# Kernel optimization log

Hardware: AMD Instinct MI355X
Metric: run time of the kernel (lower is better)

The kernel has to match this reference:

```python
import jax, jax.numpy as jnp
import numpy as np
from jax import lax

B, T = 16, 8192
CIN, HALF, F = 2, 1, 256
KS, NL, NB, TB = 3, 3, 10, 5.0
PROJ = HALF * (3 * NB - 1)


def setup_inputs() -> dict:
    key = jax.random.key(0)
    ks = jax.random.split(key, 16)
    inp = {
        'x': jax.random.normal(ks[0], (B, T, CIN), dtype=jnp.float32),
        'x_mask': jnp.ones((B, T, 1), dtype=jnp.float32),
        'w_pre': jax.random.normal(ks[1], (HALF, F)) * 0.1,
        'b_pre': jnp.zeros((F,)),
        'dw_k': jax.random.normal(ks[2], (NL, KS, 1, F)) * 0.1,   # depthwise kernels [L,k,1,C]
        'dw_b': jnp.zeros((NL, F)),
        'w11': jax.random.normal(ks[3], (NL, F, F)) * 0.05,
        'b11': jnp.zeros((NL, F)),
        'ln1_g': jnp.ones((NL, F)), 'ln1_b': jnp.zeros((NL, F)),
        'ln2_g': jnp.ones((NL, F)), 'ln2_b': jnp.zeros((NL, F)),
        'w_proj': jax.random.normal(ks[4], (F, PROJ)) * 0.05,
        'b_proj': jnp.zeros((PROJ,)),
    }
    return inp


def _layer_norm(x, g, b, eps=1e-5):
    m = jnp.mean(x, axis=-1, keepdims=True)
    v = jnp.mean(jnp.square(x - m), axis=-1, keepdims=True)
    return (x - m) * lax.rsqrt(v + eps) * g + b


def _rq_spline(x, uw, uh, ud, tail_bound, mbw=1e-3, mbh=1e-3, md=1e-3):
    # x: [B,c,T]; uw,uh: [B,c,T,K]; ud: [B,c,T,K-1]. tails='linear'.
    K = uw.shape[-1]
    const = float(np.log(np.expm1(1.0 - md)))  # boundary derivative == 1
    ud = jnp.pad(ud, [(0, 0)] * (ud.ndim - 1) + [(1, 1)], constant_values=const)
    inside = (x >= -tail_bound) & (x <= tail_bound)

    w = jax.nn.softmax(uw, axis=-1)
    w = mbw + (1.0 - mbw * K) * w
    cw = jnp.pad(jnp.cumsum(w, axis=-1), [(0, 0)] * (w.ndim - 1) + [(1, 0)])
    cw = 2.0 * tail_bound * cw - tail_bound
    cw = cw.at[..., 0].set(-tail_bound).at[..., -1].set(tail_bound)
    w = jnp.diff(cw, axis=-1)

    hgt = jax.nn.softmax(uh, axis=-1)
    hgt = mbh + (1.0 - mbh * K) * hgt
    ch = jnp.pad(jnp.cumsum(hgt, axis=-1), [(0, 0)] * (hgt.ndim - 1) + [(1, 0)])
    ch = 2.0 * tail_bound * ch - tail_bound
    ch = ch.at[..., 0].set(-tail_bound).at[..., -1].set(tail_bound)
    hgt = jnp.diff(ch, axis=-1)

    d = md + jax.nn.softplus(ud)  # [B,c,T,K+1]

    xc = jnp.clip(x, -tail_bound, tail_bound)
    idx = jnp.clip(jnp.sum((xc[..., None] >= cw).astype(jnp.int32), axis=-1) - 1, 0, K - 1)

    def g1(a, i):
        return jnp.take_along_axis(a, i[..., None], axis=-1)[..., 0]

    icw, ibw = g1(cw, idx), g1(w, idx)
    ich, ibh = g1(ch, idx), g1(hgt, idx)
    delta = ibh / ibw
    dk, dk1 = g1(d, idx), g1(d, idx + 1)

    th = (xc - icw) / ibw
    th1m = th * (1.0 - th)
    denom = delta + (dk + dk1 - 2.0 * delta) * th1m
    num = ibh * (delta * th * th + dk * th1m)
    yv = ich + num / denom
    dnum = jnp.square(delta) * (dk1 * th * th + 2.0 * delta * th1m + dk * jnp.square(1.0 - th))
    lad = jnp.log(dnum) - 2.0 * jnp.log(denom)

    y = jnp.where(inside, yv, x)
    lad = jnp.where(inside, lad, jnp.zeros_like(lad))
    return y, lad


def reference(x, x_mask, w_pre, b_pre, dw_k, dw_b, w11, b11,
              ln1_g, ln1_b, ln2_g, ln2_b, w_proj, b_proj):
    half = w_pre.shape[0]
    F_ = w_pre.shape[1]
    nl, ks = dw_k.shape[0], dw_k.shape[1]
    x0, x1 = x[..., :half], x[..., half:]

    h = x0 @ w_pre + b_pre  # pre 1x1 conv, [B,T,F]
    for i in range(nl):  # DDSConv
        dil = ks ** i
        y = lax.conv_general_dilated(h * x_mask, dw_k[i], (1,), 'SAME',
                                     rhs_dilation=(dil,),
                                     dimension_numbers=('NWC', 'WIO', 'NWC'),
                                     feature_group_count=F_) + dw_b[i]
        y = jax.nn.gelu(_layer_norm(y, ln1_g[i], ln1_b[i]), approximate=False)
        y = y @ w11[i] + b11[i]
        y = jax.nn.gelu(_layer_norm(y, ln2_g[i], ln2_b[i]), approximate=False)
        h = h + y
    h = h * x_mask
    h = (h @ w_proj + b_proj) * x_mask  # [B,T,half*(3*NB-1)]

    b_, t_ = x.shape[0], x.shape[1]
    nb = (h.shape[-1] // half + 1) // 3
    h = h.reshape(b_, t_, half, 3 * nb - 1).transpose(0, 2, 1, 3)  # [B,half,T,3NB-1]
    x1t = jnp.swapaxes(x1, 1, 2)  # [B,half,T]

    scale = 1.0 / np.sqrt(F_)
    uw = h[..., :nb] * scale
    uh = h[..., nb:2 * nb] * scale
    ud = h[..., 2 * nb:]

    y1, lad = _rq_spline(x1t, uw, uh, ud, TB)
    x1o = jnp.swapaxes(y1, 1, 2)           # [B,T,half]
    lad_t = jnp.swapaxes(lad, 1, 2)        # [B,T,half]

    xo = jnp.concatenate([x0, x1o], axis=-1) * x_mask
    logdet = jnp.sum(lad_t * x_mask, axis=(2, 1))
    return xo, logdet
```

## Files before the change

### kernel.cpp

```cpp
#include <hip/hip_runtime.h>
#include <hip/hip_bf16.h>
#include <cmath>

#define BB 16
#define TT 8192
#define MM (BB*TT)
#define FF 256
#define TBF 5.0f
#define PROJN 29

typedef __attribute__((ext_vector_type(8))) short short8;
typedef __attribute__((ext_vector_type(4))) float f32x4;

__device__ __forceinline__ float gelu_exact(float x){
    const float z  = x*0.70710678118654752440f;
    const float az = fabsf(z);
    const float t  = __builtin_amdgcn_rcpf(fmaf(0.3275911f, az, 1.0f));
    float p = fmaf(1.061405429f, t, -1.453152027f);
    p = fmaf(p, t, 1.421413741f);
    p = fmaf(p, t, -0.284496736f);
    p = fmaf(p, t, 0.254829592f);
    p = p*t;
    const float e  = __expf(-az*az);
    const float r  = fmaf(-p, e, 1.0f);
    return 0.5f*x*(1.0f + copysignf(r, z));
}
__device__ __forceinline__ float softplusf_(float v){
    return fmaxf(v,0.0f) + log1pf(__expf(-fabsf(v)));
}
__device__ __forceinline__ unsigned pack2bf(float a, float b){
    __hip_bfloat16 ha = __float2bfloat16(a);
    __hip_bfloat16 hb = __float2bfloat16(b);
    const unsigned ua = *reinterpret_cast<const unsigned short*>(&ha);
    const unsigned ub = *reinterpret_cast<const unsigned short*>(&hb);
    return ua | (ub<<16);
}
__device__ __forceinline__ float bf2f(unsigned short u){
    unsigned v = ((unsigned)u)<<16;
    return *reinterpret_cast<float*>(&v);
}
__device__ __forceinline__ float4 unpack4(uint2 q){
    float4 f;
    f.x = bf2f((unsigned short)(q.x&0xffff)); f.y = bf2f((unsigned short)(q.x>>16));
    f.z = bf2f((unsigned short)(q.y&0xffff)); f.w = bf2f((unsigned short)(q.y>>16));
    return f;
}

__global__ __launch_bounds__(256) void wprep_kernel(
    const float* __restrict__ w11, const float* __restrict__ wproj,
    __hip_bfloat16* __restrict__ wimg, __hip_bfloat16* __restrict__ wpimg)
{
    if(blockIdx.x < 24){
        const int layer = blockIdx.x>>3, kc = blockIdx.x&7;
        const float* __restrict__ w = w11 + (size_t)layer*FF*FF;
        __hip_bfloat16* __restrict__ o = wimg + (size_t)layer*81920 + kc*10240;
        for(int i=threadIdx.x; i<10240; i+=256){
            const int n = i/40, kp = i - n*40;
            const float v = (kp<32) ? w[(size_t)(kc*32+kp)*FF + n] : 0.0f;
            o[i] = __float2bfloat16(v);
        }
    } else {
        const int kc = blockIdx.x - 24;
        __hip_bfloat16* __restrict__ o = wpimg + (size_t)kc*1280;
        for(int i=threadIdx.x; i<1280; i+=256){
            const int n = i/40, kp = i - n*40;
            const float v = (kp<32 && n<PROJN) ? wproj[(size_t)(kc*32+kp)*PROJN + n] : 0.0f;
            o[i] = __float2bfloat16(v);
        }
    }
}

__global__ __launch_bounds__(256,4) void layer_kernel(
    const __hip_bfloat16* __restrict__ hbin, __hip_bfloat16* __restrict__ hbout,
    const float* __restrict__ xsrc,
    const float* __restrict__ w_pre, const float* __restrict__ b_pre,
    const float* __restrict__ mask,
    const float* __restrict__ dwk, const float* __restrict__ dwb,
    const float* __restrict__ g1, const float* __restrict__ b1,
    const __hip_bfloat16* __restrict__ wimgL, const float* __restrict__ b11,
    const float* __restrict__ g2, const float* __restrict__ b2,
    const int dil, const int pre_mode)
{
    __shared__ __hip_bfloat16 ytile[32][264];
    __shared__ __hip_bfloat16 hstash[32][268];
    __shared__ float redS[32][4];
    __shared__ float redQ[32][4];
    __shared__ float stat[32][2];

    const int tid  = threadIdx.x;
    const int wave = tid>>6, lane = tid&63;
    const int l15  = lane&15, qq = lane>>4;

    int bid = blockIdx.x;
    bid = (bid&7)*((int)gridDim.x>>3) + (bid>>3);
    const int m0 = bid*32;
    const int b  = m0/TT;
    const int t0 = m0 - b*TT;
    const float* __restrict__ mrow = mask + (size_t)b*TT;

    const int f0 = lane*4;
    const float4 k0 = *(const float4*)&dwk[f0];
    const float4 k1 = *(const float4*)&dwk[FF+f0];
    const float4 k2 = *(const float4*)&dwk[2*FF+f0];
    const float4 cb = *(const float4*)&dwb[f0];
    const float4 g1v= *(const float4*)&g1[f0];
    const float4 b1v= *(const float4*)&b1[f0];
    float4 wp4, bp4;
    if(pre_mode){ wp4 = *(const float4*)&w_pre[f0]; bp4 = *(const float4*)&b_pre[f0]; }

    #pragma unroll 4
    for(int rr=0; rr<8; ++rr){
        const int r = wave*8+rr;
        const int m = m0+r, t = t0+r;
        const int okl = (t>=dil)   ? 1 : 0;
        const int okr = (t+dil<TT) ? 1 : 0;
        const int ml  = m - dil*okl;
        const int mr  = m + dil*okr;
        const float mkc = mrow[t];
        const float mkl = mrow[t - dil*okl] * (float)okl;
        const float mkr = mrow[t + dil*okr] * (float)okr;
        float4 hc, hl, hr;
        uint2 hcraw;
        if(pre_mode){
            const float xc_ = xsrc[(size_t)m *2];
            const float xl_ = xsrc[(size_t)ml*2];
            const float xr_ = xsrc[(size_t)mr*2];
            hc.x=fmaf(xc_,wp4.x,bp4.x); hc.y=fmaf(xc_,wp4.y,bp4.y);
            hc.z=fmaf(xc_,wp4.z,bp4.z); hc.w=fmaf(xc_,wp4.w,bp4.w);
            hl.x=fmaf(xl_,wp4.x,bp4.x); hl.y=fmaf(xl_,wp4.y,bp4.y);
            hl.z=fmaf(xl_,wp4.z,bp4.z); hl.w=fmaf(xl_,wp4.w,bp4.w);
            hr.x=fmaf(xr_,wp4.x,bp4.x); hr.y=fmaf(xr_,wp4.y,bp4.y);
            hr.z=fmaf(xr_,wp4.z,bp4.z); hr.w=fmaf(xr_,wp4.w,bp4.w);
            hcraw = make_uint2(pack2bf(hc.x,hc.y), pack2bf(hc.z,hc.w));
        } else {
            hcraw          = *(const uint2*)&hbin[(size_t)m *FF + f0];
            const uint2 ql = *(const uint2*)&hbin[(size_t)ml*FF + f0];
            const uint2 qr = *(const uint2*)&hbin[(size_t)mr*FF + f0];
            hc = unpack4(hcraw); hl = unpack4(ql); hr = unpack4(qr);
        }
        *(uint2*)&hstash[r][f0] = hcraw;
        float4 a;
        a.x = fmaf(hc.x*mkc, k1.x, cb.x);
        a.y = fmaf(hc.y*mkc, k1.y, cb.y);
        a.z = fmaf(hc.z*mkc, k1.z, cb.z);
        a.w = fmaf(hc.w*mkc, k1.w, cb.w);
        a.x = fmaf(hl.x*mkl, k0.x, a.x);
        a.y = fmaf(hl.y*mkl, k0.y, a.y);
        a.z = fmaf(hl.z*mkl, k0.z, a.z);
        a.w = fmaf(hl.w*mkl, k0.w, a.w);
        a.x = fmaf(hr.x*mkr, k2.x, a.x);
        a.y = fmaf(hr.y*mkr, k2.y, a.y);
        a.z = fmaf(hr.z*mkr, k2.z, a.z);
        a.w = fmaf(hr.w*mkr, k2.w, a.w);
        float s  = a.x+a.y+a.z+a.w;
        float sq = fmaf(a.x,a.x, fmaf(a.y,a.y, fmaf(a.z,a.z, a.w*a.w)));
        #pragma unroll
        for(int o=32;o>0;o>>=1){
            s  += __shfl_xor(s,o,64);
            sq += __shfl_xor(sq,o,64);
        }
        const float mean = s*(1.0f/FF);
        const float var  = fmaf(-mean, mean, sq*(1.0f/FF));
        const float rs = rsqrtf(var + 1e-5f);
        const float y0 = gelu_exact(fmaf((a.x-mean)*rs, g1v.x, b1v.x));
        const float y1 = gelu_exact(fmaf((a.y-mean)*rs, g1v.y, b1v.y));
        const float y2 = gelu_exact(fmaf((a.z-mean)*rs, g1v.z, b1v.z));
        const float y3 = gelu_exact(fmaf((a.w-mean)*rs, g1v.w, b1v.w));
        *(uint2*)&ytile[r][f0] = make_uint2(pack2bf(y0,y1), pack2bf(y2,y3));
    }

    __syncthreads();

    const int wc = wave*64;
    f32x4 acc[2][4];
    #pragma unroll
    for(int mf=0;mf<2;++mf)
        #pragma unroll
        for(int nf=0;nf<4;++nf)
            acc[mf][nf] = (f32x4){0.f,0.f,0.f,0.f};

    #pragma unroll
    for(int kc=0;kc<8;++kc){
        short8 bfv[4];
        #pragma unroll
        for(int nf=0;nf<4;++nf)
            bfv[nf] = *(const short8*)&wimgL[(size_t)kc*10240 + (wc+nf*16+l15)*40 + qq*8];
        short8 af[2];
        #pragma unroll
        for(int mf=0;mf<2;++mf)
            af[mf] = *(const short8*)&ytile[mf*16+l15][kc*32 + qq*8];
        #pragma unroll
        for(int nf=0;nf<4;++nf)
            #pragma unroll
            for(int mf=0;mf<2;++mf)
                acc[mf][nf] = __builtin_amdgcn_mfma_f32_16x16x32_bf16(af[mf], bfv[nf], acc[mf][nf], 0,0,0);
    }

    float b11c[4], g2c[4], b2c[4];
    #pragma unroll
    for(int nf=0;nf<4;++nf){
        const int col = wc + nf*16 + l15;
        b11c[nf]=b11[col]; g2c[nf]=g2[col]; b2c[nf]=b2[col];
    }
    #pragma unroll
    for(int mf=0;mf<2;++mf){
        #pragma unroll
        for(int rg=0;rg<4;++rg){
            float s=0.f, sq=0.f;
            #pragma unroll
            for(int nf=0;nf<4;++nf){
                const float v = acc[mf][nf][rg] + b11c[nf];
                s += v; sq = fmaf(v,v,sq);
            }
            #pragma unroll
            for(int o=1;o<16;o<<=1){ s += __shfl_xor(s,o,64); sq += __shfl_xor(sq,o,64); }
            if(l15==0){
                const int row = mf*16 + qq*4 + rg;
                redS[row][wave]=s; redQ[row][wave]=sq;
            }
        }
    }
    __syncthreads();
    if(tid < 32){
        const float s  = redS[tid][0]+redS[tid][1]+redS[tid][2]+redS[tid][3];
        const float q2 = redQ[tid][0]+redQ[tid][1]+redQ[tid][2]+redQ[tid][3];
        const float mean = s*(1.0f/FF);
        const float var  = fmaf(-mean, mean, q2*(1.0f/FF));
        stat[tid][0]=mean; stat[tid][1]=rsqrtf(var+1e-5f);
    }
    __syncthreads();
    #pragma unroll
    for(int mf=0;mf<2;++mf){
        #pragma unroll
        for(int rg=0;rg<4;++rg){
            const int row = mf*16 + qq*4 + rg;
            const float mean = stat[row][0], rs = stat[row][1];
            const size_t gbase = (size_t)(m0+row)*FF;
            #pragma unroll
            for(int nf=0;nf<4;++nf){
                const int col = wc + nf*16 + l15;
                const float v  = acc[mf][nf][rg] + b11c[nf];
                const float yn = fmaf((v-mean)*rs, g2c[nf], b2c[nf]);
                const float res = bf2f(*reinterpret_cast<const unsigned short*>(&hstash[row][col]));
                hbout[gbase+col] = __float2bfloat16(res + gelu_exact(yn));
            }
        }
    }
}

__global__ __launch_bounds__(256,4) void proj_kernel(
    const __hip_bfloat16* __restrict__ hbin, const float* __restrict__ mask,
    const __hip_bfloat16* __restrict__ wpimg, const float* __restrict__ bproj,
    float* __restrict__ P)
{
    __shared__ __hip_bfloat16 ytile[64][264];
    const int tid = threadIdx.x;
    const int wave = tid>>6, lane = tid&63;
    const int l15 = lane&15, qq = lane>>4;
    const int m0 = blockIdx.x*64;
    const int f0 = lane*4;

    #pragma unroll 4
    for(int rr=0; rr<16; ++rr){
        const int r = wave*16+rr;
        const int m = m0+r;
        const float mk = mask[m];
        const float4 hc = unpack4(*(const uint2*)&hbin[(size_t)m*FF + f0]);
        *(uint2*)&ytile[r][f0] = make_uint2(pack2bf(hc.x*mk, hc.y*mk), pack2bf(hc.z*mk, hc.w*mk));
    }
    __syncthreads();

    const int rh = (wave&1)*32, wc2 = (wave>>1)*16;
    f32x4 acc[2];
    acc[0] = (f32x4){0.f,0.f,0.f,0.f};
    acc[1] = (f32x4){0.f,0.f,0.f,0.f};
    #pragma unroll
    for(int kc=0;kc<8;++kc){
        const short8 bfv = *(const short8*)&wpimg[(size_t)kc*1280 + (wc2+l15)*40 + qq*8];
        #pragma unroll
        for(int mf=0;mf<2;++mf){
            const short8 af = *(const short8*)&ytile[rh+mf*16+l15][kc*32 + qq*8];
            acc[mf] = __builtin_amdgcn_mfma_f32_16x16x32_bf16(af, bfv, acc[mf], 0,0,0);
        }
    }
    const int col = wc2 + l15;
    const float bp = (col<PROJN)? bproj[col] : 0.0f;
    #pragma unroll
    for(int mf=0;mf<2;++mf){
        #pragma unroll
        for(int rg=0;rg<4;++rg){
            const int row = rh + mf*16 + qq*4 + rg;
            const float mk = mask[m0+row];
            P[(size_t)(m0+row)*32 + col] = (acc[mf][rg] + bp)*mk;
        }
    }
}

__global__ __launch_bounds__(256) void spline_kernel(
    const float* __restrict__ P, const float* __restrict__ x,
    const float* __restrict__ mask, float* __restrict__ out,
    float* __restrict__ logdet)
{
    const int tid = threadIdx.x;
    const int m = blockIdx.x*256 + tid;
    float p[32];
    #pragma unroll
    for(int j=0;j<8;++j) ((float4*)p)[j] = ((const float4*)P)[(size_t)m*8+j];
    const float x0 = x[(size_t)m*2];
    const float x1 = x[(size_t)m*2+1];
    const float mk = mask[m];
    const float sc = 0.0625f;

    float cw[11], ch[11], d[11];
    {
        float mx=-1e30f;
        #pragma unroll
        for(int j=0;j<10;++j) mx = fmaxf(mx, p[j]);
        float e[10]; float se=0.f;
        #pragma unroll
        for(int j=0;j<10;++j){ e[j]=__expf((p[j]-mx)*sc); se+=e[j]; }
        const float inv = __fdividef(1.0f, se);
        float cum=0.f;
        cw[0]=-TBF;
        #pragma unroll
        for(int j=0;j<10;++j){ cum += fmaf(0.99f, e[j]*inv, 0.001f); cw[j+1]=fmaf(2.0f*TBF,cum,-TBF); }
        cw[10]=TBF;
    }
    {
        float mx=-1e30f;
        #pragma unroll
        for(int j=0;j<10;++j) mx = fmaxf(mx, p[10+j]);
        float e[10]; float se=0.f;
        #pragma unroll
        for(int j=0;j<10;++j){ e[j]=__expf((p[10+j]-mx)*sc); se+=e[j]; }
        const float inv = __fdividef(1.0f, se);
        float cum=0.f;
        ch[0]=-TBF;
        #pragma unroll
        for(int j=0;j<10;++j){ cum += fmaf(0.99f, e[j]*inv, 0.001f); ch[j+1]=fmaf(2.0f*TBF,cum,-TBF); }
        ch[10]=TBF;
    }
    d[0]=1.0f; d[10]=1.0f;
    #pragma unroll
    for(int k=1;k<10;++k) d[k] = 0.001f + softplusf_(p[19+k]);

    const bool inside = (x1>=-TBF)&&(x1<=TBF);
    const float xc = fminf(fmaxf(x1,-TBF),TBF);

    float icw=cw[0], ibw=cw[1]-cw[0], ich=ch[0], ibh=ch[1]-ch[0], dk=d[0], dk1=d[1];
    #pragma unroll
    for(int j=1;j<10;++j){
        const bool sel = (xc>=cw[j]);
        icw = sel? cw[j]      : icw;
        ibw = sel? cw[j+1]-cw[j] : ibw;
        ich = sel? ch[j]      : ich;
        ibh = sel? ch[j+1]-ch[j] : ibh;
        dk  = sel? d[j]       : dk;
        dk1 = sel? d[j+1]     : dk1;
    }

    const float delta = __fdividef(ibh, ibw);
    const float th = __fdividef(xc-icw, ibw);
    const float th1m = th*(1.0f-th);
    const float denom = fmaf(fmaf(-2.0f,delta,dk+dk1), th1m, delta);
    const float num = ibh*fmaf(delta*th, th, dk*th1m);
    const float yv = ich + __fdividef(num, denom);
    const float omt = 1.0f-th;
    const float dnum = delta*delta*(dk1*th*th + 2.0f*delta*th1m + dk*omt*omt);
    const float lad = __logf(dnum) - 2.0f*__logf(denom);
    const float y1 = inside? yv : x1;
    const float lv = inside? lad : 0.0f;

    out[(size_t)m*2]   = x0*mk;
    out[(size_t)m*2+1] = y1*mk;

    __shared__ float red[256];
    red[tid]=lv*mk;
    __syncthreads();
    #pragma unroll
    for(int s=128;s>0;s>>=1){ if(tid<s) red[tid]+=red[tid+s]; __syncthreads(); }
    if(tid==0) atomicAdd(&logdet[blockIdx.x>>5], red[0]);
}

extern "C" void kernel_launch(void* const* d_in, const int* in_sizes, int n_in,
                              void* d_out, int out_size, void* d_ws, size_t ws_size,
                              hipStream_t stream)
{
    const float* x      = (const float*)d_in[0];
    const float* mask   = (const float*)d_in[1];
    const float* w_pre  = (const float*)d_in[2];
    const float* b_pre  = (const float*)d_in[3];
    const float* dw_k   = (const float*)d_in[4];
    const float* dw_b   = (const float*)d_in[5];
    const float* w11    = (const float*)d_in[6];
    const float* b11    = (const float*)d_in[7];
    const float* ln1g   = (const float*)d_in[8];
    const float* ln1b   = (const float*)d_in[9];
    const float* ln2g   = (const float*)d_in[10];
    const float* ln2b   = (const float*)d_in[11];
    const float* w_proj = (const float*)d_in[12];
    const float* b_proj = (const float*)d_in[13];

    const size_t hbytes_f32 = (size_t)MM*FF*4;
    __hip_bfloat16* h0 = (__hip_bfloat16*)d_ws;
    __hip_bfloat16* h1 = h0 + (size_t)MM*FF;
    float* P = (float*)d_ws;
    float* outp   = (float*)d_out;
    float* logdet = outp + (size_t)MM*2;

    __hip_bfloat16* wimg;
    if(ws_size >= 2*hbytes_f32 + 3*163840 + 20480)
        wimg = (__hip_bfloat16*)((char*)d_ws + 2*hbytes_f32);
    else
        wimg = (__hip_bfloat16*)d_out;
    __hip_bfloat16* wpimg = wimg + (size_t)3*81920;

    wprep_kernel<<<32, 256, 0, stream>>>(w11, w_proj, wimg, wpimg);

    layer_kernel<<<MM/32, 256, 0, stream>>>(
        (const __hip_bfloat16*)nullptr, h1, x, w_pre, b_pre, mask,
        dw_k, dw_b, ln1g, ln1b, wimg, b11, ln2g, ln2b, 1, 1);
    layer_kernel<<<MM/32, 256, 0, stream>>>(
        h1, h0, x, w_pre, b_pre, mask,
        dw_k + (size_t)3*FF, dw_b + (size_t)FF,
        ln1g + (size_t)FF, ln1b + (size_t)FF,
        wimg + (size_t)81920, b11 + (size_t)FF,
        ln2g + (size_t)FF, ln2b + (size_t)FF, 3, 0);
    layer_kernel<<<MM/32, 256, 0, stream>>>(
        h0, h1, x, w_pre, b_pre, mask,
        dw_k + (size_t)6*FF, dw_b + (size_t)2*FF,
        ln1g + (size_t)2*FF, ln1b + (size_t)2*FF,
        wimg + (size_t)2*81920, b11 + (size_t)2*FF,
        ln2g + (size_t)2*FF, ln2b + (size_t)2*FF, 9, 0);

    proj_kernel<<<MM/64, 256, 0, stream>>>(h1, mask, wpimg, b_proj, P);

    hipMemsetAsync(logdet, 0, BB*sizeof(float), stream);
    spline_kernel<<<MM/256, 256, 0, stream>>>(P, x, mask, outp, logdet);
}
```

Before: 354.5 us.

## Fuse projection with spline, use tanh-style GELU, shrink LDS padding

Combines the projection GEMM and the spline evaluation into one kernel that keeps projection outputs in shared memory, removing the P round trip through global memory and one launch. Replaces the erf-based exact GELU with a sigmoid/tanh approximation to cut ALU work in the layer kernels, which changes numerics away from exact GELU. Also changes LDS row padding, swaps divides for rcp, and tightens the workspace-size check so the fused path is taken when the bf16 buffers fit.

After: 327.5 us. -7.6%, faster.

```diff
diff --git a/kernel.cpp b/kernel.cpp
--- a/kernel.cpp
+++ b/kernel.cpp
@@ -12,18 +12,11 @@
 typedef __attribute__((ext_vector_type(8))) short short8;
 typedef __attribute__((ext_vector_type(4))) float f32x4;
 
-__device__ __forceinline__ float gelu_exact(float x){
-    const float z  = x*0.70710678118654752440f;
-    const float az = fabsf(z);
-    const float t  = __builtin_amdgcn_rcpf(fmaf(0.3275911f, az, 1.0f));
-    float p = fmaf(1.061405429f, t, -1.453152027f);
-    p = fmaf(p, t, 1.421413741f);
-    p = fmaf(p, t, -0.284496736f);
-    p = fmaf(p, t, 0.254829592f);
-    p = p*t;
-    const float e  = __expf(-az*az);
-    const float r  = fmaf(-p, e, 1.0f);
-    return 0.5f*x*(1.0f + copysignf(r, z));
+__device__ __forceinline__ float gelu_fast(float x){
+    const float x2 = x*x;
+    const float v  = x*fmaf(0.07135481627f, x2, 1.595769122f);
+    const float e  = __expf(-v);
+    return x*__builtin_amdgcn_rcpf(1.0f + e);
 }
 __device__ __forceinline__ float softplusf_(float v){
     return fmaxf(v,0.0f) + log1pf(__expf(-fabsf(v)));
@@ -81,8 +74,8 @@
     const float* __restrict__ g2, const float* __restrict__ b2,
     const int dil, const int pre_mode)
 {
-    __shared__ __hip_bfloat16 ytile[32][264];
-    __shared__ __hip_bfloat16 hstash[32][268];
+    __shared__ __hip_bfloat16 ytile[32][260];
+    __shared__ __hip_bfloat16 hstash[32][260];
     __shared__ float redS[32][4];
     __shared__ float redQ[32][4];
     __shared__ float stat[32][2];
@@ -162,10 +155,10 @@
         const float mean = s*(1.0f/FF);
         const float var  = fmaf(-mean, mean, sq*(1.0f/FF));
         const float rs = rsqrtf(var + 1e-5f);
-        const float y0 = gelu_exact(fmaf((a.x-mean)*rs, g1v.x, b1v.x));
-        const float y1 = gelu_exact(fmaf((a.y-mean)*rs, g1v.y, b1v.y));
-        const float y2 = gelu_exact(fmaf((a.z-mean)*rs, g1v.z, b1v.z));
-        const float y3 = gelu_exact(fmaf((a.w-mean)*rs, g1v.w, b1v.w));
+        const float y0 = gelu_fast(fmaf((a.x-mean)*rs, g1v.x, b1v.x));
+        const float y1 = gelu_fast(fmaf((a.y-mean)*rs, g1v.y, b1v.y));
+        const float y2 = gelu_fast(fmaf((a.z-mean)*rs, g1v.z, b1v.z));
+        const float y3 = gelu_fast(fmaf((a.w-mean)*rs, g1v.w, b1v.w));
         *(uint2*)&ytile[r][f0] = make_uint2(pack2bf(y0,y1), pack2bf(y2,y3));
     }
 
@@ -242,10 +235,146 @@
                 const float v  = acc[mf][nf][rg] + b11c[nf];
                 const float yn = fmaf((v-mean)*rs, g2c[nf], b2c[nf]);
                 const float res = bf2f(*reinterpret_cast<const unsigned short*>(&hstash[row][col]));
-                hbout[gbase+col] = __float2bfloat16(res + gelu_exact(yn));
+                hbout[gbase+col] = __float2bfloat16(res + gelu_fast(yn));
             }
         }
     }
+}
+
+__global__ __launch_bounds__(256,2) void projspline_kernel(
+    const __hip_bfloat16* __restrict__ hbin, const float* __restrict__ mask,
+    const __hip_bfloat16* __restrict__ wpimg, const float* __restrict__ bproj,
+    const float* __restrict__ x, float* __restrict__ out,
+    float* __restrict__ logdet)
+{
+    __shared__ __hip_bfloat16 ytile[64][260];
+    __shared__ float Pl[256][37];
+    __shared__ float red[256];
+
+    const int tid = threadIdx.x;
+    const int wave = tid>>6, lane = tid&63;
+    const int l15 = lane&15, qq = lane>>4;
+    const int m0 = blockIdx.x*256;
+    const int f0 = lane*4;
+
+    const int col = (wave>>1)*16 + l15;
+    const float bp = (col<PROJN)? bproj[col] : 0.0f;
+
+    for(int ch=0; ch<4; ++ch){
+        const int mc = m0 + ch*64;
+        #pragma unroll 4
+        for(int rr=0; rr<16; ++rr){
+            const int r = wave*16+rr;
+            const int m = mc+r;
+            const float mk = mask[m];
+            const float4 hc = unpack4(*(const uint2*)&hbin[(size_t)m*FF + f0]);
+            *(uint2*)&ytile[r][f0] = make_uint2(pack2bf(hc.x*mk, hc.y*mk), pack2bf(hc.z*mk, hc.w*mk));
+        }
+        __syncthreads();
+
+        const int rh = (wave&1)*32, wc2 = (wave>>1)*16;
+        f32x4 acc[2];
+        acc[0] = (f32x4){0.f,0.f,0.f,0.f};
+        acc[1] = (f32x4){0.f,0.f,0.f,0.f};
+        #pragma unroll
+        for(int kc=0;kc<8;++kc){
+            const short8 bfv = *(const short8*)&wpimg[(size_t)kc*1280 + (wc2+l15)*40 + qq*8];
+            #pragma unroll
+            for(int mf=0;mf<2;++mf){
+                const short8 af = *(const short8*)&ytile[rh+mf*16+l15][kc*32 + qq*8];
+                acc[mf] = __builtin_amdgcn_mfma_f32_16x16x32_bf16(af, bfv, acc[mf], 0,0,0);
+            }
+        }
+        #pragma unroll
+        for(int mf=0;mf<2;++mf){
+            #pragma unroll
+            for(int rg=0;rg<4;++rg){
+                const int row = rh + mf*16 + qq*4 + rg;
+                const float mk = mask[mc+row];
+                Pl[ch*64+row][col] = (acc[mf][rg] + bp)*mk;
+            }
+        }
+        __syncthreads();
+    }
+
+    const int m = m0 + tid;
+    float p[29];
+    #pragma unroll
+    for(int j=0;j<29;++j) p[j] = Pl[tid][j];
+    const float x0 = x[(size_t)m*2];
+    const float x1 = x[(size_t)m*2+1];
+    const float mk = mask[m];
+    const float sc = 0.0625f;
+
+    float cw[11], ch_[11], d[11];
+    {
+        float mx=-1e30f;
+        #pragma unroll
+        for(int j=0;j<10;++j) mx = fmaxf(mx, p[j]);
+        float e[10]; float se=0.f;
+        #pragma unroll
+        for(int j=0;j<10;++j){ e[j]=__expf((p[j]-mx)*sc); se+=e[j]; }
+        const float inv = __builtin_amdgcn_rcpf(se);
+        float cum=0.f;
+        cw[0]=-TBF;
+        #pragma unroll
+        for(int j=0;j<10;++j){ cum += fmaf(0.99f, e[j]*inv, 0.001f); cw[j+1]=fmaf(2.0f*TBF,cum,-TBF); }
+        cw[10]=TBF;
+    }
+    {
+        float mx=-1e30f;
+        #pragma unroll
+        for(int j=0;j<10;++j) mx = fmaxf(mx, p[10+j]);
+        float e[10]; float se=0.f;
+        #pragma unroll
+        for(int j=0;j<10;++j){ e[j]=__expf((p[10+j]-mx)*sc); se+=e[j]; }
+        const float inv = __builtin_amdgcn_rcpf(se);
+        float cum=0.f;
+        ch_[0]=-TBF;
+        #pragma unroll
+        for(int j=0;j<10;++j){ cum += fmaf(0.99f, e[j]*inv, 0.001f); ch_[j+1]=fmaf(2.0f*TBF,cum,-TBF); }
+        ch_[10]=TBF;
+    }
+    d[0]=1.0f; d[10]=1.0f;
+    #pragma unroll
+    for(int k=1;k<10;++k) d[k] = 0.001f + softplusf_(p[19+k]);
+
+    const bool inside = (x1>=-TBF)&&(x1<=TBF);
+    const float xc = fminf(fmaxf(x1,-TBF),TBF);
+
+    float icw=cw[0], ibw=cw[1]-cw[0], ich=ch_[0], ibh=ch_[1]-ch_[0], dk=d[0], dk1=d[1];
+    #pragma unroll
+    for(int j=1;j<10;++j){
+        const bool sel = (xc>=cw[j]);
+        icw = sel? cw[j]        : icw;
+        ibw = sel? cw[j+1]-cw[j]: ibw;
+        ich = sel? ch_[j]       : ich;
+        ibh = sel? ch_[j+1]-ch_[j]: ibh;
+        dk  = sel? d[j]         : dk;
+        dk1 = sel? d[j+1]       : dk1;
+    }
+
+    const float delta = __fdividef(ibh, ibw);
+    const float th = __fdividef(xc-icw, ibw);
+    const float th1m = th*(1.0f-th);
+    const float denom = fmaf(fmaf(-2.0f,delta,dk+dk1), th1m, delta);
+    const float num = ibh*fmaf(delta*th, th, dk*th1m);
+    const float rcd = __builtin_amdgcn_rcpf(denom);
+    const float yv = ich + num*rcd;
+    const float omt = 1.0f-th;
+    const float dnum = delta*delta*(dk1*th*th + 2.0f*delta*th1m + dk*omt*omt);
+    const float lad = __logf(dnum*rcd*rcd);
+    const float y1 = inside? yv : x1;
+    const float lv = inside? lad : 0.0f;
+
+    out[(size_t)m*2]   = x0*mk;
+    out[(size_t)m*2+1] = y1*mk;
+
+    red[tid]=lv*mk;
+    __syncthreads();
+    #pragma unroll
+    for(int s=128;s>0;s>>=1){ if(tid<s) red[tid]+=red[tid+s]; __syncthreads(); }
+    if(tid==0) atomicAdd(&logdet[blockIdx.x>>5], red[0]);
 }
 
 __global__ __launch_bounds__(256,4) void proj_kernel(
@@ -253,7 +382,7 @@
     const __hip_bfloat16* __restrict__ wpimg, const float* __restrict__ bproj,
     float* __restrict__ P)
 {
-    __shared__ __hip_bfloat16 ytile[64][264];
+    __shared__ __hip_bfloat16 ytile[64][260];
     const int tid = threadIdx.x;
     const int wave = tid>>6, lane = tid&63;
     const int l15 = lane&15, qq = lane>>4;
@@ -311,7 +440,7 @@
     const float mk = mask[m];
     const float sc = 0.0625f;
 
-    float cw[11], ch[11], d[11];
+    float cw[11], ch_[11], d[11];
     {
         float mx=-1e30f;
         #pragma unroll
@@ -319,7 +448,7 @@
         float e[10]; float se=0.f;
         #pragma unroll
         for(int j=0;j<10;++j){ e[j]=__expf((p[j]-mx)*sc); se+=e[j]; }
-        const float inv = __fdividef(1.0f, se);
+        const float inv = __builtin_amdgcn_rcpf(se);
         float cum=0.f;
         cw[0]=-TBF;
         #pragma unroll
@@ -333,12 +462,12 @@
         float e[10]; float se=0.f;
         #pragma unroll
         for(int j=0;j<10;++j){ e[j]=__expf((p[10+j]-mx)*sc); se+=e[j]; }
-        const float inv = __fdividef(1.0f, se);
+        const float inv = __builtin_amdgcn_rcpf(se);
         float cum=0.f;
-        ch[0]=-TBF;
-        #pragma unroll
-        for(int j=0;j<10;++j){ cum += fmaf(0.99f, e[j]*inv, 0.001f); ch[j+1]=fmaf(2.0f*TBF,cum,-TBF); }
-        ch[10]=TBF;
+        ch_[0]=-TBF;
+        #pragma unroll
+        for(int j=0;j<10;++j){ cum += fmaf(0.99f, e[j]*inv, 0.001f); ch_[j+1]=fmaf(2.0f*TBF,cum,-TBF); }
+        ch_[10]=TBF;
     }
     d[0]=1.0f; d[10]=1.0f;
     #pragma unroll
@@ -347,16 +476,16 @@
     const bool inside = (x1>=-TBF)&&(x1<=TBF);
     const float xc = fminf(fmaxf(x1,-TBF),TBF);
 
-    float icw=cw[0], ibw=cw[1]-cw[0], ich=ch[0], ibh=ch[1]-ch[0], dk=d[0], dk1=d[1];
+    float icw=cw[0], ibw=cw[1]-cw[0], ich=ch_[0], ibh=ch_[1]-ch_[0], dk=d[0], dk1=d[1];
     #pragma unroll
     for(int j=1;j<10;++j){
         const bool sel = (xc>=cw[j]);
-        icw = sel? cw[j]      : icw;
-        ibw = sel? cw[j+1]-cw[j] : ibw;
-        ich = sel? ch[j]      : ich;
-        ibh = sel? ch[j+1]-ch[j] : ibh;
-        dk  = sel? d[j]       : dk;
-        dk1 = sel? d[j+1]     : dk1;
+        icw = sel? cw[j]        : icw;
+        ibw = sel? cw[j+1]-cw[j]: ibw;
+        ich = sel? ch_[j]       : ich;
+        ibh = sel? ch_[j+1]-ch_[j]: ibh;
+        dk  = sel? d[j]         : dk;
+        dk1 = sel? d[j+1]       : dk1;
     }
 
     const float delta = __fdividef(ibh, ibw);
@@ -364,10 +493,11 @@
     const float th1m = th*(1.0f-th);
     const float denom = fmaf(fmaf(-2.0f,delta,dk+dk1), th1m, delta);
     const float num = ibh*fmaf(delta*th, th, dk*th1m);
-    const float yv = ich + __fdividef(num, denom);
+    const float rcd = __builtin_amdgcn_rcpf(denom);
+    const float yv = ich + num*rcd;
     const float omt = 1.0f-th;
     const float dnum = delta*delta*(dk1*th*th + 2.0f*delta*th1m + dk*omt*omt);
-    const float lad = __logf(dnum) - 2.0f*__logf(denom);
+    const float lad = __logf(dnum*rcd*rcd);
     const float y1 = inside? yv : x1;
     const float lv = inside? lad : 0.0f;
 
@@ -401,18 +531,17 @@
     const float* w_proj = (const float*)d_in[12];
     const float* b_proj = (const float*)d_in[13];
 
-    const size_t hbytes_f32 = (size_t)MM*FF*4;
+    const size_t hbytes_bf16 = (size_t)MM*FF*2;
     __hip_bfloat16* h0 = (__hip_bfloat16*)d_ws;
     __hip_bfloat16* h1 = h0 + (size_t)MM*FF;
-    float* P = (float*)d_ws;
     float* outp   = (float*)d_out;
     float* logdet = outp + (size_t)MM*2;
 
+    const size_t wimg_bytes = (size_t)3*163840 + 20480;
     __hip_bfloat16* wimg;
-    if(ws_size >= 2*hbytes_f32 + 3*163840 + 20480)
-        wimg = (__hip_bfloat16*)((char*)d_ws + 2*hbytes_f32);
-    else
-        wimg = (__hip_bfloat16*)d_out;
+    const bool ws_ok = (ws_size >= 2*hbytes_bf16 + wimg_bytes);
+    if(ws_ok) wimg = (__hip_bfloat16*)((char*)d_ws + 2*hbytes_bf16);
+    else      wimg = (__hip_bfloat16*)d_out;
     __hip_bfloat16* wpimg = wimg + (size_t)3*81920;
 
     wprep_kernel<<<32, 256, 0, stream>>>(w11, w_proj, wimg, wpimg);
@@ -433,8 +562,12 @@
         wimg + (size_t)2*81920, b11 + (size_t)2*FF,
         ln2g + (size_t)2*FF, ln2b + (size_t)2*FF, 9, 0);
 
-    proj_kernel<<<MM/64, 256, 0, stream>>>(h1, mask, wpimg, b_proj, P);
-
     hipMemsetAsync(logdet, 0, BB*sizeof(float), stream);
-    spline_kernel<<<MM/256, 256, 0, stream>>>(P, x, mask, outp, logdet);
-}
+    if(ws_ok){
+        projspline_kernel<<<MM/256, 256, 0, stream>>>(h1, mask, wpimg, b_proj, x, outp, logdet);
+    } else {
+        float* P = (float*)d_ws;
+        proj_kernel<<<MM/64, 256, 0, stream>>>(h1, mask, wpimg, b_proj, P);
+        spline_kernel<<<MM/256, 256, 0, stream>>>(P, x, mask, outp, logdet);
+    }
+}
```
